# Kernel tuning notes

Hardware: AMD Instinct MI355X
Metric: run time of the kernel (lower is better)

Reference implementation:

```python
import jax, jax.numpy as jnp
import numpy as np

ALPHA = 1.0
BETA = 1.0
N_TDA = 16      # n: points subsampled per diagram
Q = 2.0         # Wasserstein order
NN_SIZE = 5     # knn size (self + 4 neighbors)
RADIUS = 0.07
H = 0.03
EPS = 1e-12
B, N = 8, 4096


def _sqdist(a, b):
    # a: [..., M, 3], b: [..., K, 3] -> [..., M, K] squared Euclidean distances
    aa = jnp.sum(a * a, -1)[..., :, None]
    bb = jnp.sum(b * b, -1)[..., None, :]
    ab = jnp.einsum('...md,...kd->...mk', a, b)
    return aa + bb - 2.0 * ab


def _mst_deaths(pts):
    # H0 persistence of Vietoris-Rips complex: births all 0, finite deaths are
    # the edge weights of the MST of the complete graph (Prim's algorithm).
    n = pts.shape[0]
    d = jnp.sqrt(jnp.maximum(_sqdist(pts, pts), 0.0))  # [n, n]
    in_tree = jnp.zeros((n,), bool).at[0].set(True)
    mind = d[0]  # distance from each node to the current tree

    def step(carry, _):
        in_tree, mind = carry
        m = jnp.where(in_tree, jnp.inf, mind)
        j = jnp.argmin(m)
        w = m[j]
        in_tree = in_tree.at[j].set(True)
        mind = jnp.minimum(mind, d[j])
        return (in_tree, mind), w

    _, deaths = jax.lax.scan(step, (in_tree, mind), None, length=n - 1)
    return deaths  # [n-1]


def _forward(pred, gt, pcd_radius):
    b = pred.shape[0]
    # ---- EMD loss (nearest-neighbor surrogate of CUDA auction_match) ----
    cost = _sqdist(pred, gt)                              # [B, N, N]
    idx = jnp.argmin(cost, axis=-1)                       # [B, N]
    matched = jnp.take_along_axis(gt, idx[..., None], axis=1)
    d2 = jnp.mean(((pred - matched) ** 2).reshape(b, -1), axis=1, keepdims=True)
    emd = jnp.mean(d2 / pcd_radius)
    # ---- Repulsion loss ----
    dpp = _sqdist(pred, pred)                             # [B, N, N]
    _, knn = jax.lax.top_k(-dpp, NN_SIZE)                 # nearest incl. self
    knn = knn[:, :, 1:]                                   # drop self -> [B, N, 4]
    grouped = jax.vmap(lambda p, ix: p[ix])(pred, knn)    # [B, N, 4, 3]
    r2 = jnp.maximum(jnp.sum((grouped - pred[:, :, None, :]) ** 2, -1), EPS)
    dist = jnp.sqrt(r2)
    rep = jnp.mean((RADIUS - dist) * jnp.exp(-r2 / H ** 2))
    # ---- TDA loss (per-sample VR H0 diagram + q-Wasserstein) ----
    key = jax.random.key(42)
    kp, kg = jax.random.split(key)

    def sub(k, pts):
        ix = jax.random.permutation(k, pts.shape[0])[:N_TDA]
        return pts[ix]

    pred_s = jax.vmap(sub)(jax.random.split(kp, b), pred)  # [B, 16, 3]
    gt_s = jax.vmap(sub)(jax.random.split(kg, b), gt)
    dp = jnp.sort(jax.vmap(_mst_deaths)(pred_s), axis=-1)  # [B, 15]
    dg = jnp.sort(jax.vmap(_mst_deaths)(gt_s), axis=-1)
    wd = jnp.sum(jnp.abs(dp - dg) ** Q, axis=-1) ** (1.0 / Q)
    tda = jnp.mean(wd)
    return (emd * 100.0, rep * ALPHA, tda * BETA)


def setup_inputs() -> dict:
    key = jax.random.key(0)
    k1, k2, k3 = jax.random.split(key, 3)
    pred = jax.random.normal(k1, (B, N, 3), jnp.float32)
    gt = jax.random.normal(k2, (B, N, 3), jnp.float32)
    pcd_radius = jax.random.uniform(k3, (B, 1), jnp.float32) + 0.5
    return {"pred": pred, "gt": gt, "pcd_radius": pcd_radius}


def reference(pred, gt, pcd_radius):
    return _forward(pred, gt, pcd_radius)
```

## Files before the change

kernel.cpp:

```cpp
#include <hip/hip_runtime.h>
#include <cstdint>
#include <cmath>
#include <vector>
#include <algorithm>
#include <numeric>

#define B_SZ 8
#define N_PTS 4096
#define TBLK 256

struct TdaArgs { int idx[16][16]; };

__global__ __launch_bounds__(TBLK)
void pair_kernel(const float* __restrict__ pred, const float* __restrict__ gt,
                 double* __restrict__ acc) {
  __shared__ float4 sg[N_PTS];
  __shared__ double wred[TBLK / 64];

  const int tid   = threadIdx.x;
  const int chunk = blockIdx.x;
  const int b     = blockIdx.y;
  const int job   = blockIdx.z;

  const float* src = (job == 0 ? gt : pred) + (size_t)b * N_PTS * 3;
  for (int j = tid; j < N_PTS; j += TBLK) {
    float x = src[3 * j + 0];
    float y = src[3 * j + 1];
    float z = src[3 * j + 2];
    float nn = fmaf(x, x, fmaf(y, y, z * z));
    sg[j] = make_float4(x, y, z, -0.5f * nn);
  }
  __syncthreads();

  const int i = chunk * TBLK + tid;
  const float* pp = pred + ((size_t)b * N_PTS + i) * 3;
  const float px = pp[0], py = pp[1], pz = pp[2];
  const float pn = fmaf(px, px, fmaf(py, py, pz * pz));

  double tval;
  if (job == 0) {
    float bt = -INFINITY;
    #pragma unroll 8
    for (int j = 0; j < N_PTS; ++j) {
      float4 g = sg[j];
      float t = fmaf(px, g.x, fmaf(py, g.y, fmaf(pz, g.z, g.w)));
      bt = fmaxf(bt, t);
    }
    tval = (double)fmaf(-2.0f, bt, pn);
  } else {
    float t0 = -INFINITY, t1 = -INFINITY, t2 = -INFINITY, t3 = -INFINITY, t4 = -INFINITY;
    int   i0 = 0, i1 = 0, i2 = 0, i3 = 0, i4 = 0;
    #pragma unroll 4
    for (int j = 0; j < N_PTS; ++j) {
      float4 g = sg[j];
      float t = fmaf(px, g.x, fmaf(py, g.y, fmaf(pz, g.z, g.w)));
      if (t > t4) {
        t4 = t; i4 = j;
        if (t4 > t3) { float f = t3; t3 = t4; t4 = f; int q = i3; i3 = i4; i4 = q; }
        if (t3 > t2) { float f = t2; t2 = t3; t3 = f; int q = i2; i2 = i3; i3 = q; }
        if (t2 > t1) { float f = t1; t1 = t2; t2 = f; int q = i1; i1 = i2; i2 = q; }
        if (t1 > t0) { float f = t0; t0 = t1; t1 = f; int q = i0; i0 = i1; i1 = q; }
      }
    }
    (void)t0; (void)i0;
    double s = 0.0;
    const int nbr[4] = { i1, i2, i3, i4 };
    #pragma unroll
    for (int k = 0; k < 4; ++k) {
      float4 g = sg[nbr[k]];
      float dx = px - g.x, dy = py - g.y, dz = pz - g.z;
      float r2 = fmaxf(fmaf(dx, dx, fmaf(dy, dy, dz * dz)), 1e-12f);
      float dist = sqrtf(r2);
      s += (double)((0.07f - dist) * expf(-r2 / 9.0e-4f));
    }
    tval = s;
  }

  double v = tval;
  #pragma unroll
  for (int off = 32; off > 0; off >>= 1) v += __shfl_down(v, off);
  if ((tid & 63) == 0) wred[tid >> 6] = v;
  __syncthreads();
  if (tid == 0) {
    double s = 0.0;
    #pragma unroll
    for (int w = 0; w < TBLK / 64; ++w) s += wred[w];
    acc[job * 128 + b * 16 + chunk] = s;
  }
}

__global__ __launch_bounds__(64)
void final_kernel(const float* __restrict__ pred, const float* __restrict__ gt,
                  const float* __restrict__ pcd, const double* __restrict__ acc,
                  float* __restrict__ out, TdaArgs args) {
  __shared__ float pts[16][16][3];
  __shared__ float aa[16][16];
  __shared__ float mind[16][16];
  __shared__ float deaths[16][15];
  __shared__ float wd[8];
  const int tid = threadIdx.x;

  if (tid < 16) {
    const float* src = (tid < 8) ? (pred + (size_t)tid * N_PTS * 3)
                                 : (gt + (size_t)(tid - 8) * N_PTS * 3);
    for (int k = 0; k < 16; ++k) {
      int ix = args.idx[tid][k];
      float x = src[3 * ix + 0], y = src[3 * ix + 1], z = src[3 * ix + 2];
      pts[tid][k][0] = x; pts[tid][k][1] = y; pts[tid][k][2] = z;
      aa[tid][k] = x * x + y * y + z * z;
    }
    #define DFORM(j, k) \
      sqrtf(fmaxf(aa[tid][j] + aa[tid][k] - 2.0f * (pts[tid][j][0] * pts[tid][k][0] + \
            pts[tid][j][1] * pts[tid][k][1] + pts[tid][j][2] * pts[tid][k][2]), 0.0f))
    for (int k = 0; k < 16; ++k) mind[tid][k] = DFORM(0, k);
    unsigned mask = 1u;
    for (int step = 0; step < 15; ++step) {
      float best = INFINITY; int bj = 0;
      for (int k = 0; k < 16; ++k) {
        float m = ((mask >> k) & 1u) ? INFINITY : mind[tid][k];
        if (m < best) { best = m; bj = k; }
      }
      deaths[tid][step] = best;
      mask |= (1u << bj);
      for (int k = 0; k < 16; ++k) {
        float d = DFORM(bj, k);
        mind[tid][k] = fminf(mind[tid][k], d);
      }
    }
    #undef DFORM
    for (int a = 1; a < 15; ++a) {
      float v = deaths[tid][a];
      int c = a;
      while (c > 0 && deaths[tid][c - 1] > v) { deaths[tid][c] = deaths[tid][c - 1]; --c; }
      deaths[tid][c] = v;
    }
  }
  __syncthreads();
  if (tid < 8) {
    float s = 0.0f;
    for (int k = 0; k < 15; ++k) {
      float d = deaths[tid][k] - deaths[tid + 8][k];
      s += d * d;
    }
    wd[tid] = sqrtf(s);
  }
  __syncthreads();
  if (tid == 0) {
    double tda = 0.0;
    for (int b = 0; b < 8; ++b) tda += (double)wd[b];
    tda /= 8.0;
    double emd = 0.0;
    for (int b = 0; b < 8; ++b) {
      double s = 0.0;
      for (int c = 0; c < 16; ++c) s += acc[b * 16 + c];
      emd += (s / (double)(N_PTS * 3)) / (double)pcd[b];
    }
    emd = emd / 8.0 * 100.0;
    double rep = 0.0;
    for (int k = 0; k < 128; ++k) rep += acc[128 + k];
    rep /= (double)(B_SZ * N_PTS * 4);
    out[0] = (float)emd;
    out[1] = (float)rep;
    out[2] = (float)tda;
  }
}

static inline uint32_t rotl32(uint32_t x, int d) { return (x << d) | (x >> (32 - d)); }

static void threefry2x32_host(uint32_t k0, uint32_t k1, uint32_t& x0, uint32_t& x1) {
  const uint32_t ks[3] = { k0, k1, k0 ^ k1 ^ 0x1BD11BDAu };
  static const int rot[2][4] = { {13, 15, 26, 6}, {17, 29, 16, 24} };
  x0 += ks[0]; x1 += ks[1];
  for (int i = 0; i < 5; ++i) {
    const int* r = rot[i & 1];
    for (int j = 0; j < 4; ++j) {
      x0 += x1;
      x1 = rotl32(x1, r[j]);
      x1 ^= x0;
    }
    x0 += ks[(i + 1) % 3];
    x1 += ks[(i + 2) % 3] + (uint32_t)(i + 1);
  }
}

static void jax_split_p(const uint32_t key[2], int n, uint32_t (*out)[2]) {
  for (int j = 0; j < n; ++j) {
    uint32_t a = 0u, b = (uint32_t)j;
    threefry2x32_host(key[0], key[1], a, b);
    out[j][0] = a; out[j][1] = b;
  }
}

static void jax_bits32_p(const uint32_t key[2], int n, uint32_t* bits) {
  for (int i = 0; i < n; ++i) {
    uint32_t a = 0u, b = (uint32_t)i;
    threefry2x32_host(key[0], key[1], a, b);
    bits[i] = a ^ b;
  }
}

static void jax_perm_first16(const uint32_t key_in[2], int n, int* out16) {
  std::vector<int> x((size_t)n);
  std::iota(x.begin(), x.end(), 0);
  uint32_t key[2] = { key_in[0], key_in[1] };
  const int rounds = (int)std::ceil(3.0 * std::log((double)n) / std::log(4294967295.0));
  std::vector<uint32_t> bits((size_t)n);
  std::vector<int> ord((size_t)n), nx((size_t)n);
  for (int r = 0; r < rounds; ++r) {
    uint32_t kr[2][2];
    jax_split_p(key, 2, kr);
    key[0] = kr[0][0]; key[1] = kr[0][1];
    jax_bits32_p(kr[1], n, bits.data());
    std::iota(ord.begin(), ord.end(), 0);
    std::stable_sort(ord.begin(), ord.end(),
                     [&](int A, int Bv) { return bits[A] < bits[Bv]; });
    for (int i = 0; i < n; ++i) nx[i] = x[ord[i]];
    x.swap(nx);
  }
  for (int i = 0; i < 16; ++i) out16[i] = x[i];
}

static void compute_tda_indices(TdaArgs& args) {
  const uint32_t root[2] = { 0u, 42u };
  uint32_t kpg[2][2];
  jax_split_p(root, 2, kpg);
  uint32_t kb[B_SZ][2];
  jax_split_p(kpg[0], B_SZ, kb);
  for (int b = 0; b < B_SZ; ++b) jax_perm_first16(kb[b], N_PTS, args.idx[b]);
  jax_split_p(kpg[1], B_SZ, kb);
  for (int b = 0; b < B_SZ; ++b) jax_perm_first16(kb[b], N_PTS, args.idx[8 + b]);
}


extern "C" void kernel_launch(void* const* d_in, const int* in_sizes, int n_in,
                              void* d_out, int out_size, void* d_ws, size_t ws_size,
                              hipStream_t stream) {
  const float* pred = (const float*)d_in[0];
  const float* gt   = (const float*)d_in[1];
  const float* pcd  = (const float*)d_in[2];
  float*  out = (float*)d_out;
  double* acc = (double*)d_ws;

  TdaArgs targs;
  compute_tda_indices(targs);

  dim3 grid(N_PTS / TBLK, B_SZ, 2);
  pair_kernel<<<grid, dim3(TBLK), 0, stream>>>(pred, gt, acc);
  final_kernel<<<dim3(1), dim3(64), 0, stream>>>(pred, gt, pcd, acc, out, targs);
}
```

Before: 5.004 ms.

## Split candidate range across blocks and merge partial NN/top-k results in new kernel

```diff
diff --git a/kernel.cpp b/kernel.cpp
--- a/kernel.cpp
+++ b/kernel.cpp
@@ -8,90 +8,153 @@
 #define B_SZ 8
 #define N_PTS 4096
 #define TBLK 256
+#define NSPLIT 4
+#define JTILE (N_PTS / NSPLIT)
 
 struct TdaArgs { int idx[16][16]; };
 
-__global__ __launch_bounds__(TBLK)
+#define WS_BT(p)   ((float*)(p))
+#define WS_KNN(p)  ((int*)((char*)(p) + 0x80000))
+#define WS_PART(p) ((double*)((char*)(p) + 0x300000))
+
+__global__ __launch_bounds__(TBLK, 4)
 void pair_kernel(const float* __restrict__ pred, const float* __restrict__ gt,
-                 double* __restrict__ acc) {
-  __shared__ float4 sg[N_PTS];
-  __shared__ double wred[TBLK / 64];
+                 float* __restrict__ bt_out, int* __restrict__ knn_out) {
+  __shared__ float4 sg[JTILE];
 
   const int tid   = threadIdx.x;
   const int chunk = blockIdx.x;
   const int b     = blockIdx.y;
-  const int job   = blockIdx.z;
-
-  const float* src = (job == 0 ? gt : pred) + (size_t)b * N_PTS * 3;
-  for (int j = tid; j < N_PTS; j += TBLK) {
+  const int q     = blockIdx.z % NSPLIT;
+  const int job   = blockIdx.z / NSPLIT;
+  const int jbase = q * JTILE;
+
+  const float* src = (job == 0 ? gt : pred) + ((size_t)b * N_PTS + jbase) * 3;
+  for (int j = tid; j < JTILE; j += TBLK) {
     float x = src[3 * j + 0];
     float y = src[3 * j + 1];
     float z = src[3 * j + 2];
-    float nn = fmaf(x, x, fmaf(y, y, z * z));
-    sg[j] = make_float4(x, y, z, -0.5f * nn);
-  }
-  __syncthreads();
+    sg[j] = make_float4(x, y, z, -0.5f * fmaf(x, x, fmaf(y, y, z * z)));
+  }
 
   const int i = chunk * TBLK + tid;
   const float* pp = pred + ((size_t)b * N_PTS + i) * 3;
   const float px = pp[0], py = pp[1], pz = pp[2];
-  const float pn = fmaf(px, px, fmaf(py, py, pz * pz));
-
-  double tval;
+  __syncthreads();
+
   if (job == 0) {
     float bt = -INFINITY;
-    #pragma unroll 8
-    for (int j = 0; j < N_PTS; ++j) {
-      float4 g = sg[j];
-      float t = fmaf(px, g.x, fmaf(py, g.y, fmaf(pz, g.z, g.w)));
-      bt = fmaxf(bt, t);
-    }
-    tval = (double)fmaf(-2.0f, bt, pn);
+    for (int j0 = 0; j0 < JTILE; j0 += 8) {
+      float t[8];
+      #pragma unroll
+      for (int k = 0; k < 8; ++k) {
+        float4 g = sg[j0 + k];
+        t[k] = fmaf(px, g.x, fmaf(py, g.y, fmaf(pz, g.z, g.w)));
+      }
+      #pragma unroll
+      for (int k = 0; k < 8; ++k) bt = fmaxf(bt, t[k]);
+    }
+    bt_out[((size_t)q * B_SZ + b) * N_PTS + i] = bt;
   } else {
     float t0 = -INFINITY, t1 = -INFINITY, t2 = -INFINITY, t3 = -INFINITY, t4 = -INFINITY;
     int   i0 = 0, i1 = 0, i2 = 0, i3 = 0, i4 = 0;
-    #pragma unroll 4
-    for (int j = 0; j < N_PTS; ++j) {
-      float4 g = sg[j];
-      float t = fmaf(px, g.x, fmaf(py, g.y, fmaf(pz, g.z, g.w)));
-      if (t > t4) {
-        t4 = t; i4 = j;
-        if (t4 > t3) { float f = t3; t3 = t4; t4 = f; int q = i3; i3 = i4; i4 = q; }
-        if (t3 > t2) { float f = t2; t2 = t3; t3 = f; int q = i2; i2 = i3; i3 = q; }
-        if (t2 > t1) { float f = t1; t1 = t2; t2 = f; int q = i1; i1 = i2; i2 = q; }
-        if (t1 > t0) { float f = t0; t0 = t1; t1 = f; int q = i0; i0 = i1; i1 = q; }
-      }
-    }
-    (void)t0; (void)i0;
-    double s = 0.0;
-    const int nbr[4] = { i1, i2, i3, i4 };
+    for (int j0 = 0; j0 < JTILE; j0 += 8) {
+      float t[8];
+      #pragma unroll
+      for (int k = 0; k < 8; ++k) {
+        float4 g = sg[j0 + k];
+        t[k] = fmaf(px, g.x, fmaf(py, g.y, fmaf(pz, g.z, g.w)));
+      }
+      float gm = fmaxf(fmaxf(fmaxf(t[0], t[1]), fmaxf(t[2], t[3])),
+                       fmaxf(fmaxf(t[4], t[5]), fmaxf(t[6], t[7])));
+      if (gm > t4) {
+        #pragma unroll
+        for (int k = 0; k < 8; ++k) {
+          if (t[k] > t4) {
+            t4 = t[k]; i4 = j0 + k;
+            if (t4 > t3) { float f = t3; t3 = t4; t4 = f; int p_ = i3; i3 = i4; i4 = p_; }
+            if (t3 > t2) { float f = t2; t2 = t3; t3 = f; int p_ = i2; i2 = i3; i3 = p_; }
+            if (t2 > t1) { float f = t1; t1 = t2; t2 = f; int p_ = i1; i1 = i2; i2 = p_; }
+            if (t1 > t0) { float f = t0; t0 = t1; t1 = f; int p_ = i0; i0 = i1; i1 = p_; }
+          }
+        }
+      }
+    }
+    int* o = knn_out + (((size_t)q * B_SZ + b) * N_PTS + i) * 5;
+    o[0] = jbase + i0; o[1] = jbase + i1; o[2] = jbase + i2;
+    o[3] = jbase + i3; o[4] = jbase + i4;
+  }
+}
+
+__global__ __launch_bounds__(TBLK)
+void merge_kernel(const float* __restrict__ pred,
+                  const float* __restrict__ bt_in, const int* __restrict__ knn_in,
+                  double* __restrict__ partials) {
+  __shared__ double wred[2][TBLK / 64];
+  const int tid = threadIdx.x;
+  const int blk = blockIdx.x;
+  const int b   = blk >> 4;
+  const int i   = (blk & 15) * TBLK + tid;
+
+  const float* pb = pred + (size_t)b * N_PTS * 3;
+  const float px = pb[3 * i + 0], py = pb[3 * i + 1], pz = pb[3 * i + 2];
+  const float pn = fmaf(px, px, fmaf(py, py, pz * pz));
+
+  float bt = -INFINITY;
+  #pragma unroll
+  for (int q = 0; q < NSPLIT; ++q)
+    bt = fmaxf(bt, bt_in[((size_t)q * B_SZ + b) * N_PTS + i]);
+  double emd = (double)fmaf(-2.0f, bt, pn);
+
+  float s0 = INFINITY, s1 = INFINITY, s2 = INFINITY, s3 = INFINITY;
+  int   j0v = 0x7fffffff, j1v = 0x7fffffff, j2v = 0x7fffffff, j3v = 0x7fffffff;
+  #pragma unroll
+  for (int q = 0; q < NSPLIT; ++q) {
+    const int* kn = knn_in + (((size_t)q * B_SZ + b) * N_PTS + i) * 5;
+    #pragma unroll
+    for (int c = 0; c < 5; ++c) {
+      int idx = kn[c];
+      float gx = pb[3 * idx + 0], gy = pb[3 * idx + 1], gz = pb[3 * idx + 2];
+      float dx = px - gx, dy = py - gy, dz = pz - gz;
+      float r2 = fmaf(dx, dx, fmaf(dy, dy, dz * dz));
+      if (idx == i) r2 = INFINITY;
+      bool lt3 = (r2 < s3) || (r2 == s3 && idx < j3v);
+      if (lt3) {
+        s3 = r2; j3v = idx;
+        if ((s3 < s2) || (s3 == s2 && j3v < j2v)) { float f = s2; s2 = s3; s3 = f; int p_ = j2v; j2v = j3v; j3v = p_; }
+        if ((s2 < s1) || (s2 == s1 && j2v < j1v)) { float f = s1; s1 = s2; s2 = f; int p_ = j1v; j1v = j2v; j2v = p_; }
+        if ((s1 < s0) || (s1 == s0 && j1v < j0v)) { float f = s0; s0 = s1; s1 = f; int p_ = j0v; j0v = j1v; j1v = p_; }
+      }
+    }
+  }
+  double rep = 0.0;
+  {
+    float rr[4] = { s0, s1, s2, s3 };
     #pragma unroll
     for (int k = 0; k < 4; ++k) {
-      float4 g = sg[nbr[k]];
-      float dx = px - g.x, dy = py - g.y, dz = pz - g.z;
-      float r2 = fmaxf(fmaf(dx, dx, fmaf(dy, dy, dz * dz)), 1e-12f);
+      float r2 = fmaxf(rr[k], 1e-12f);
       float dist = sqrtf(r2);
-      s += (double)((0.07f - dist) * expf(-r2 / 9.0e-4f));
-    }
-    tval = s;
-  }
-
-  double v = tval;
+      rep += (double)((0.07f - dist) * expf(-r2 / 9.0e-4f));
+    }
+  }
+
+  double v0 = emd, v1 = rep;
   #pragma unroll
-  for (int off = 32; off > 0; off >>= 1) v += __shfl_down(v, off);
-  if ((tid & 63) == 0) wred[tid >> 6] = v;
+  for (int off = 32; off > 0; off >>= 1) { v0 += __shfl_down(v0, off); v1 += __shfl_down(v1, off); }
+  if ((tid & 63) == 0) { wred[0][tid >> 6] = v0; wred[1][tid >> 6] = v1; }
   __syncthreads();
   if (tid == 0) {
-    double s = 0.0;
+    double a = 0.0, r = 0.0;
     #pragma unroll
-    for (int w = 0; w < TBLK / 64; ++w) s += wred[w];
-    acc[job * 128 + b * 16 + chunk] = s;
+    for (int w = 0; w < TBLK / 64; ++w) { a += wred[0][w]; r += wred[1][w]; }
+    partials[blk * 2 + 0] = a;
+    partials[blk * 2 + 1] = r;
   }
 }
 
 __global__ __launch_bounds__(64)
 void final_kernel(const float* __restrict__ pred, const float* __restrict__ gt,
-                  const float* __restrict__ pcd, const double* __restrict__ acc,
+                  const float* __restrict__ pcd, const double* __restrict__ partials,
                   float* __restrict__ out, TdaArgs args) {
   __shared__ float pts[16][16][3];
   __shared__ float aa[16][16];
@@ -122,10 +185,7 @@
       }
       deaths[tid][step] = best;
       mask |= (1u << bj);
-      for (int k = 0; k < 16; ++k) {
-        float d = DFORM(bj, k);
-        mind[tid][k] = fminf(mind[tid][k], d);
-      }
+      for (int k = 0; k < 16; ++k) mind[tid][k] = fminf(mind[tid][k], DFORM(bj, k));
     }
     #undef DFORM
     for (int a = 1; a < 15; ++a) {
@@ -152,12 +212,12 @@
     double emd = 0.0;
     for (int b = 0; b < 8; ++b) {
       double s = 0.0;
-      for (int c = 0; c < 16; ++c) s += acc[b * 16 + c];
+      for (int c = 0; c < 16; ++c) s += partials[(b * 16 + c) * 2];
       emd += (s / (double)(N_PTS * 3)) / (double)pcd[b];
     }
     emd = emd / 8.0 * 100.0;
     double rep = 0.0;
-    for (int k = 0; k < 128; ++k) rep += acc[128 + k];
+    for (int k = 0; k < 128; ++k) rep += partials[k * 2 + 1];
     rep /= (double)(B_SZ * N_PTS * 4);
     out[0] = (float)emd;
     out[1] = (float)rep;
@@ -238,13 +298,16 @@
   const float* pred = (const float*)d_in[0];
   const float* gt   = (const float*)d_in[1];
   const float* pcd  = (const float*)d_in[2];
-  float*  out = (float*)d_out;
-  double* acc = (double*)d_ws;
+  float* out = (float*)d_out;
 
   TdaArgs targs;
   compute_tda_indices(targs);
 
-  dim3 grid(N_PTS / TBLK, B_SZ, 2);
-  pair_kernel<<<grid, dim3(TBLK), 0, stream>>>(pred, gt, acc);
-  final_kernel<<<dim3(1), dim3(64), 0, stream>>>(pred, gt, pcd, acc, out, targs);
-}
+  float*  bt   = WS_BT(d_ws);
+  int*    knn  = WS_KNN(d_ws);
+  double* part = WS_PART(d_ws);
+
+  pair_kernel<<<dim3(N_PTS / TBLK, B_SZ, 2 * NSPLIT), dim3(TBLK), 0, stream>>>(pred, gt, bt, knn);
+  merge_kernel<<<dim3(B_SZ * N_PTS / TBLK), dim3(TBLK), 0, stream>>>(pred, bt, knn, part);
+  final_kernel<<<dim3(1), dim3(64), 0, stream>>>(pred, gt, pcd, part, out, targs);
+}
```

New measurement: 4.762 ms. -4.8%, faster.
